# Optimization experiments

Hardware: AMD Instinct MI355X
Metric: run time of the kernel (lower is better)

Reference implementation:

```python
import jax, jax.numpy as jnp
import numpy as np

N, NPER, B, E = 65536, 1024, 64, 1048576
IN_F, HID, K, NCLS = 128, 64, 16, 10


def setup_inputs() -> dict:
    key = jax.random.key(0)
    ks = jax.random.split(key, 12)
    x = jax.random.normal(ks[0], (N, IN_F), jnp.float32)
    # block-structured intra-graph edges: 64 graphs of 1024 contiguous nodes
    gid = jax.random.randint(ks[1], (E,), 0, B)
    src = gid * NPER + jax.random.randint(ks[2], (E,), 0, NPER)
    dst = gid * NPER + jax.random.randint(ks[3], (E,), 0, NPER)
    edge_index = jnp.stack([src, dst]).astype(jnp.int32)
    batch = (jnp.arange(N, dtype=jnp.int32) // NPER).astype(jnp.int32)
    def lin(k, fo, fi):
        kw, kb = jax.random.split(k)
        s = 1.0 / np.sqrt(fi)
        return (jax.random.uniform(kw, (fo, fi), jnp.float32, -s, s),
                jax.random.uniform(kb, (fo,), jnp.float32, -s, s))
    W1, b1 = lin(ks[4], HID, IN_F)
    W2, b2 = lin(ks[5], HID, HID)
    Wp, bp = lin(ks[6], K, HID)      # DMoN cluster-assignment MLP (single Linear)
    Wl, bl = lin(ks[7], NCLS, HID)   # final classifier
    return {"x": x, "edge_index": edge_index, "batch": batch,
            "W1": W1, "b1": b1, "W2": W2, "b2": b2,
            "Wp": Wp, "bp": bp, "Wl": Wl, "bl": bl}


def gcn_conv(x, src, dst, W, b):
    # GCNConv with add_self_loops=True, symmetric normalization
    n = x.shape[0]
    deg = jax.ops.segment_sum(jnp.ones(src.shape[0], x.dtype), dst,
                              num_segments=n) + 1.0  # +1 for self-loop
    dinv = jax.lax.rsqrt(deg)
    h = x @ W.T
    coef = (dinv[src] * dinv[dst])[:, None]
    agg = jax.ops.segment_sum(h[src] * coef, dst, num_segments=n)
    agg = agg + h * (dinv * dinv)[:, None]  # self-loop contribution
    return agg + b


def reference(x, edge_index, batch, W1, b1, W2, b2, Wp, bp, Wl, bl):
    src, dst = edge_index[0], edge_index[1]
    h = jax.nn.relu(gcn_conv(x, src, dst, W1, b1))
    h = jax.nn.relu(gcn_conv(h, src, dst, W2, b2))
    # to_dense_batch: graphs are equal-sized and contiguous -> reshape, mask all True
    Xb = h.reshape(B, NPER, HID)
    # DMoN cluster assignment (dropout=0.0, mask all ones)
    s = jax.nn.softmax(Xb @ Wp.T + bp, axis=-1)          # [B, NPER, K]
    Xp = jax.nn.selu(jnp.einsum('bnk,bnh->bkh', s, Xb))   # pooled clusters [B, K, HID]
    out = Xp.mean(axis=1)                                  # [B, HID]
    logits = out @ Wl.T + bl                               # [B, NCLS]
    return logits
```

## Files before the change

### kernel.cpp

```cpp
#include <hip/hip_runtime.h>
#include <cstddef>

#define N_NODES 65536
#define NPER    1024
#define NGRAPH  64
#define HID     64
#define IN_F    128
#define KCLUS   16
#define NCLS    10
#define ECAP    20480
#define HSTRIDE 12
#define ZROW    NPER
#define LIN_BLOCKS 512

template <int K>
__device__ __forceinline__ void gemm_tile(const float* __restrict__ X,
                                          const float* __restrict__ W,
                                          float* __restrict__ Y,
                                          float (*xs)[68], float (*ws)[68],
                                          int block, int t) {
    const size_t row0 = (size_t)block * 128;
    const int rbase = t >> 3;
    const int cbase = t & 7;
    float acc[4][8] = {};

    for (int kc = 0; kc < K; kc += 64) {
        __syncthreads();
        for (int i = t; i < 128 * 16; i += 256) {
            int row = i >> 4, k4 = (i & 15) << 2;
            *(float4*)&xs[row][k4] = *(const float4*)(X + (row0 + row) * K + kc + k4);
        }
        for (int i = t; i < 64 * 16; i += 256) {
            int col = i >> 4, k4 = (i & 15) << 2;
            *(float4*)&ws[col][k4] = *(const float4*)(W + col * K + kc + k4);
        }
        __syncthreads();

#pragma unroll 4
        for (int k4 = 0; k4 < 64; k4 += 4) {
            float4 xr[4], wr[8];
#pragma unroll
            for (int rr = 0; rr < 4; ++rr) xr[rr] = *(const float4*)&xs[rbase + 32 * rr][k4];
#pragma unroll
            for (int cc = 0; cc < 8; ++cc) wr[cc] = *(const float4*)&ws[cbase + 8 * cc][k4];
#pragma unroll
            for (int rr = 0; rr < 4; ++rr)
#pragma unroll
                for (int cc = 0; cc < 8; ++cc) {
                    acc[rr][cc] = fmaf(xr[rr].x, wr[cc].x, acc[rr][cc]);
                    acc[rr][cc] = fmaf(xr[rr].y, wr[cc].y, acc[rr][cc]);
                    acc[rr][cc] = fmaf(xr[rr].z, wr[cc].z, acc[rr][cc]);
                    acc[rr][cc] = fmaf(xr[rr].w, wr[cc].w, acc[rr][cc]);
                }
        }
    }

#pragma unroll
    for (int rr = 0; rr < 4; ++rr)
#pragma unroll
        for (int cc = 0; cc < 8; ++cc)
            Y[(row0 + rbase + 32 * rr) * HID + cbase + 8 * cc] = acc[rr][cc];
}

__global__ __launch_bounds__(256) void front_kernel(const float* __restrict__ X,
                                                    const float* __restrict__ W,
                                                    float* __restrict__ Y,
                                                    const int* __restrict__ src,
                                                    const int* __restrict__ dst,
                                                    int* __restrict__ ecnt,
                                                    int* __restrict__ gedges, int E) {
    __shared__ float xs[128][68];
    __shared__ float ws[64][68];
    const int t = threadIdx.x;

    if (blockIdx.x >= LIN_BLOCKS) {
        int* hist = (int*)&xs[0][0];
        int* base_l = hist + NGRAPH;
        const int e0 = (blockIdx.x - LIN_BLOCKS) * 1024;
        if (t < NGRAPH) hist[t] = 0;
        __syncthreads();

        int gg[4], rr[4], pk[4];
#pragma unroll
        for (int i = 0; i < 4; ++i) {
            int idx = e0 + i * 256 + t;
            if (idx < E) {
                int d = dst[idx], s = src[idx];
                int g = d >> 10;
                gg[i] = g;
                pk[i] = ((d & 1023) << 10) | (s & 1023);
                rr[i] = atomicAdd(&hist[g], 1);
            } else gg[i] = -1;
        }
        __syncthreads();
        if (t < NGRAPH) base_l[t] = atomicAdd(&ecnt[t], hist[t]);
        __syncthreads();
#pragma unroll
        for (int i = 0; i < 4; ++i) {
            if (gg[i] >= 0) {
                int pos = base_l[gg[i]] + rr[i];
                if (pos < ECAP) gedges[gg[i] * ECAP + pos] = pk[i];
            }
        }
        return;
    }

    gemm_tile<IN_F>(X, W, Y, xs, ws, blockIdx.x, t);
}

template <int K>
__global__ __launch_bounds__(256) void linear_kernel(const float* __restrict__ X,
                                                     const float* __restrict__ W,
                                                     float* __restrict__ Y) {
    __shared__ float xs[128][68];
    __shared__ float ws[64][68];
    gemm_tile<K>(X, W, Y, xs, ws, blockIdx.x, threadIdx.x);
}

__global__ __launch_bounds__(1024) void scatter_kernel(const int* __restrict__ gedges,
                                                       const int* __restrict__ ecnt,
                                                       int* __restrict__ rp,
                                                       unsigned short* __restrict__ esorted,
                                                       float* __restrict__ dinv) {
    __shared__ int hist[NPER];
    __shared__ int wsum[16];
    const int g = blockIdx.x >> 3;
    const int sub = blockIdx.x & 7;
    const int t = threadIdx.x;
    const int lane = t & 63, wid = t >> 6;
    const int ec = ecnt[g];
    const int* ge = gedges + (size_t)g * ECAP;

    hist[t] = 0;
    __syncthreads();
    for (int i = t; i < ec; i += 1024) atomicAdd(&hist[ge[i] >> 10], 1);
    __syncthreads();

    const int h0 = hist[t];
    const int pd = (h0 + 3) & ~3;
    int v = pd;
#pragma unroll
    for (int off = 1; off < 64; off <<= 1) {
        int x = __shfl_up(v, off, 64);
        if (lane >= off) v += x;
    }
    if (lane == 63) wsum[wid] = v;
    __syncthreads();
    if (wid == 0) {
        int wv = (lane < 16) ? wsum[lane] : 0;
#pragma unroll
        for (int off = 1; off < 16; off <<= 1) {
            int x = __shfl_up(wv, off, 64);
            if (lane >= off) wv += x;
        }
        if (lane < 16) wsum[lane] = wv;
    }
    __syncthreads();
    const int incl = v + (wid > 0 ? wsum[wid - 1] : 0);
    const int excl = incl - pd;

    if (sub == 0) {
        rp[g * (NPER + 1) + t] = excl;
        if (t == NPER - 1) rp[g * (NPER + 1) + NPER] = incl;
        dinv[g * NPER + t] = rsqrtf((float)h0 + 1.0f);
    }
    __syncthreads();
    hist[t] = excl;
    __syncthreads();

    unsigned short* es = esorted + (size_t)g * ECAP;

    if ((t >> 7) == sub)
        for (int q = excl + h0; q < excl + pd; ++q) es[q] = (unsigned short)ZROW;

    for (int i = t; i < ec; i += 1024) {
        int pk = ge[i];
        int d = pk >> 10;
        if ((d >> 7) == sub) {
            int pos = atomicAdd(&hist[d], 1);
            es[pos] = (unsigned short)(pk & 1023);
        }
    }
}

__global__ __launch_bounds__(512) void agg_kernel(const float* __restrict__ h,
                                                  const unsigned short* __restrict__ esorted,
                                                  const int* __restrict__ rp,
                                                  const float* __restrict__ dinv,
                                                  const float* __restrict__ bias,
                                                  float* __restrict__ outp) {
    __shared__ float Hs[(NPER + 1) * HSTRIDE];
    __shared__ float dl[NPER];
    const int g = blockIdx.x & 63;
    const int f0 = (blockIdx.x >> 6) * 8;
    const int t = threadIdx.x;
    const int base = g * NPER;

    for (int r = t; r < NPER; r += 512) {
        const float* hp = h + (size_t)(base + r) * HID + f0;
        float4 a = *(const float4*)hp;
        float4 b = *(const float4*)(hp + 4);
        float dv = dinv[base + r];
        dl[r] = dv;
        float* row = &Hs[r * HSTRIDE];
        *(float4*)row = make_float4(a.x * dv, a.y * dv, a.z * dv, a.w * dv);
        *(float4*)(row + 4) = make_float4(b.x * dv, b.y * dv, b.z * dv, b.w * dv);
    }
    if (t < HSTRIDE) Hs[ZROW * HSTRIDE + t] = 0.f;
    float bb[8];
#pragma unroll
    for (int j = 0; j < 8; ++j) bb[j] = bias[f0 + j];
    const unsigned short* es = esorted + (size_t)g * ECAP;
    const int* rpg = rp + g * (NPER + 1);
    __syncthreads();

    for (int ld = t; ld < NPER; ld += 512) {
        int p = rpg[ld];
        const int pe = rpg[ld + 1];
        const float* srow = &Hs[ld * HSTRIDE];
        float4 acc0 = *(const float4*)srow;
        float4 acc1 = *(const float4*)(srow + 4);
        float4 bcc0 = make_float4(0.f, 0.f, 0.f, 0.f);
        float4 bcc1 = make_float4(0.f, 0.f, 0.f, 0.f);

        for (; p < pe; p += 4) {
            uint2 w4 = *(const uint2*)(es + p);
            const float* r0 = &Hs[(int)(w4.x & 0xFFFFu) * HSTRIDE];
            const float* r1 = &Hs[(int)(w4.x >> 16) * HSTRIDE];
            const float* r2 = &Hs[(int)(w4.y & 0xFFFFu) * HSTRIDE];
            const float* r3 = &Hs[(int)(w4.y >> 16) * HSTRIDE];
            float4 a0 = *(const float4*)r0, a1 = *(const float4*)(r0 + 4);
            float4 b0 = *(const float4*)r1, b1 = *(const float4*)(r1 + 4);
            float4 c0v = *(const float4*)r2, c1v = *(const float4*)(r2 + 4);
            float4 d0 = *(const float4*)r3, d1 = *(const float4*)(r3 + 4);
            acc0.x += a0.x; acc0.y += a0.y; acc0.z += a0.z; acc0.w += a0.w;
            acc1.x += a1.x; acc1.y += a1.y; acc1.z += a1.z; acc1.w += a1.w;
            bcc0.x += b0.x; bcc0.y += b0.y; bcc0.z += b0.z; bcc0.w += b0.w;
            bcc1.x += b1.x; bcc1.y += b1.y; bcc1.z += b1.z; bcc1.w += b1.w;
            acc0.x += c0v.x; acc0.y += c0v.y; acc0.z += c0v.z; acc0.w += c0v.w;
            acc1.x += c1v.x; acc1.y += c1v.y; acc1.z += c1v.z; acc1.w += c1v.w;
            bcc0.x += d0.x; bcc0.y += d0.y; bcc0.z += d0.z; bcc0.w += d0.w;
            bcc1.x += d1.x; bcc1.y += d1.y; bcc1.z += d1.z; bcc1.w += d1.w;
        }
        acc0.x += bcc0.x; acc0.y += bcc0.y; acc0.z += bcc0.z; acc0.w += bcc0.w;
        acc1.x += bcc1.x; acc1.y += bcc1.y; acc1.z += bcc1.z; acc1.w += bcc1.w;

        const float dv = dl[ld];
        float4 o0, o1;
        o0.x = fmaxf(fmaf(acc0.x, dv, bb[0]), 0.f);
        o0.y = fmaxf(fmaf(acc0.y, dv, bb[1]), 0.f);
        o0.z = fmaxf(fmaf(acc0.z, dv, bb[2]), 0.f);
        o0.w = fmaxf(fmaf(acc0.w, dv, bb[3]), 0.f);
        o1.x = fmaxf(fmaf(acc1.x, dv, bb[4]), 0.f);
        o1.y = fmaxf(fmaf(acc1.y, dv, bb[5]), 0.f);
        o1.z = fmaxf(fmaf(acc1.z, dv, bb[6]), 0.f);
        o1.w = fmaxf(fmaf(acc1.w, dv, bb[7]), 0.f);
        float* op = outp + (size_t)(base + ld) * HID + f0;
        *(float4*)op = o0;
        *(float4*)(op + 4) = o1;
    }
}

__global__ __launch_bounds__(256) void pool1_kernel(const float* __restrict__ h,
                                                    const float* __restrict__ Wp,
                                                    const float* __restrict__ bp,
                                                    float* __restrict__ xpart) {
    __shared__ float xs[128][HID + 1];
    __shared__ float ss[128][KCLUS + 1];
    __shared__ float wp[KCLUS][HID];
    __shared__ float bps[KCLUS];
    const int g = blockIdx.x >> 3;
    const int c = blockIdx.x & 7;
    const int t = threadIdx.x;
    const float* hb = h + ((size_t)g * NPER + c * 128) * HID;

    for (int i = t; i < 128 * HID / 4; i += 256) {
        float4 v = ((const float4*)hb)[i];
        int row = i >> 4, col = (i & 15) * 4;
        xs[row][col] = v.x; xs[row][col + 1] = v.y; xs[row][col + 2] = v.z; xs[row][col + 3] = v.w;
    }
    for (int i = t; i < KCLUS * HID; i += 256) wp[i >> 6][i & 63] = Wp[i];
    if (t < KCLUS) bps[t] = bp[t];
    __syncthreads();

    if (t < 128) {
        float lg[KCLUS];
        float mx = -1e30f;
#pragma unroll
        for (int k = 0; k < KCLUS; ++k) {
            float a = bps[k];
#pragma unroll 8
            for (int hh = 0; hh < HID; ++hh) a = fmaf(xs[t][hh], wp[k][hh], a);
            lg[k] = a;
            mx = fmaxf(mx, a);
        }
        float sum = 0.f;
#pragma unroll
        for (int k = 0; k < KCLUS; ++k) {
            lg[k] = __expf(lg[k] - mx);
            sum += lg[k];
        }
        float inv = 1.0f / sum;
#pragma unroll
        for (int k = 0; k < KCLUS; ++k) ss[t][k] = lg[k] * inv;
    }
    __syncthreads();

    const int hcol = t & 63;
    const int k0 = (t >> 6) * 4;
    float a0 = 0.f, a1 = 0.f, a2 = 0.f, a3 = 0.f;
#pragma unroll 8
    for (int n = 0; n < 128; ++n) {
        float xv = xs[n][hcol];
        a0 = fmaf(ss[n][k0 + 0], xv, a0);
        a1 = fmaf(ss[n][k0 + 1], xv, a1);
        a2 = fmaf(ss[n][k0 + 2], xv, a2);
        a3 = fmaf(ss[n][k0 + 3], xv, a3);
    }
    float* xp = xpart + (((size_t)(g * 8 + c)) * KCLUS + k0) * HID + hcol;
    xp[0] = a0; xp[HID] = a1; xp[2 * HID] = a2; xp[3 * HID] = a3;
}

__global__ __launch_bounds__(256) void pool2_kernel(const float* __restrict__ xpart,
                                                    const float* __restrict__ Wl,
                                                    const float* __restrict__ bl,
                                                    float* __restrict__ out) {
    __shared__ float xp[KCLUS][HID + 1];
    __shared__ float outm[HID];
    const int g = blockIdx.x;
    const int t = threadIdx.x;
    const int hcol = t & 63;
    const int k0 = (t >> 6) * 4;
    const float* base = xpart + (size_t)g * 8 * KCLUS * HID;

    float a[4] = {};
#pragma unroll
    for (int c = 0; c < 8; ++c)
#pragma unroll
        for (int j = 0; j < 4; ++j)
            a[j] += base[(c * KCLUS + k0 + j) * HID + hcol];

    const float sc = 1.0507009873554805f, al = 1.6732632423543772f;
#pragma unroll
    for (int j = 0; j < 4; ++j) {
        float v = a[j];
        xp[k0 + j][hcol] = v > 0.f ? sc * v : sc * al * (__expf(v) - 1.f);
    }
    __syncthreads();

    if (t < HID) {
        float m = 0.f;
#pragma unroll
        for (int k = 0; k < KCLUS; ++k) m += xp[k][t];
        outm[t] = m * (1.0f / KCLUS);
    }
    __syncthreads();

    if (t < NCLS) {
        float acc = bl[t];
#pragma unroll 8
        for (int hh = 0; hh < HID; ++hh) acc = fmaf(outm[hh], Wl[t * HID + hh], acc);
        out[g * NCLS + t] = acc;
    }
}

extern "C" void kernel_launch(void* const* d_in, const int* in_sizes, int n_in,
                              void* d_out, int out_size, void* d_ws, size_t ws_size,
                              hipStream_t stream) {
    const float* x  = (const float*)d_in[0];
    const int* eidx = (const int*)d_in[1];
    const float* W1 = (const float*)d_in[3];
    const float* b1 = (const float*)d_in[4];
    const float* W2 = (const float*)d_in[5];
    const float* b2 = (const float*)d_in[6];
    const float* Wp = (const float*)d_in[7];
    const float* bp = (const float*)d_in[8];
    const float* Wl = (const float*)d_in[9];
    const float* bl = (const float*)d_in[10];
    float* out = (float*)d_out;

    const int E = in_sizes[1] / 2;
    const int* src = eidx;
    const int* dst = eidx + E;

    char* w = (char*)d_ws;
    int*            ecnt    = (int*)w;            w += 256;
    int*            gedges  = (int*)w;            w += (size_t)NGRAPH * ECAP * 4;
    unsigned short* esorted = (unsigned short*)w; w += (size_t)NGRAPH * ECAP * 2;
    int*            rp      = (int*)w;            w += (size_t)NGRAPH * (NPER + 1) * 4;
    float*          dinv    = (float*)w;          w += (size_t)N_NODES * 4;
    float*          A       = (float*)w;          w += (size_t)N_NODES * HID * 4;
    float*          Bf      = (float*)w;          w += (size_t)N_NODES * HID * 4;
    float*          xpart   = (float*)w;          w += (size_t)NGRAPH * 8 * KCLUS * HID * 4;

    hipMemsetAsync(ecnt, 0, 256, stream);

    const int nbucket = (E + 1023) / 1024;
    front_kernel<<<LIN_BLOCKS + nbucket, 256, 0, stream>>>(x, W1, A, src, dst, ecnt, gedges, E);

    scatter_kernel<<<NGRAPH * 8, 1024, 0, stream>>>(gedges, ecnt, rp, esorted, dinv);

    agg_kernel<<<NGRAPH * 8, 512, 0, stream>>>(A, esorted, rp, dinv, b1, Bf);

    linear_kernel<HID><<<N_NODES / 128, 256, 0, stream>>>(Bf, W2, A);
    agg_kernel<<<NGRAPH * 8, 512, 0, stream>>>(A, esorted, rp, dinv, b2, Bf);

    pool1_kernel<<<NGRAPH * 8, 256, 0, stream>>>(Bf, Wp, bp, xpart);
    pool2_kernel<<<NGRAPH, 256, 0, stream>>>(xpart, Wl, bl, out);
}
```

Before: 218.0 us.

## Fuse node linear transforms into GCN aggregation kernels

Removes the standalone tiled GEMM kernels and computes each node's 8-feature slice of X·Wᵀ inside the aggregation kernel, just before staging it into shared memory. This drops the round trip of the transformed feature matrix through global memory and one kernel launch per layer. In exchange, each of the 8 feature-slice blocks per graph rereads the full input rows (128 or 64 floats per node), so input reads grow about eightfold. The GEMM also becomes a per-thread scalar dot-product loop with weights held in shared memory instead of a register-blocked tile.

```diff
diff --git a/kernel.cpp b/kernel.cpp
--- a/kernel.cpp
+++ b/kernel.cpp
@@ -11,110 +11,40 @@
 #define ECAP    20480
 #define HSTRIDE 12
 #define ZROW    NPER
-#define LIN_BLOCKS 512
-
-template <int K>
-__device__ __forceinline__ void gemm_tile(const float* __restrict__ X,
-                                          const float* __restrict__ W,
-                                          float* __restrict__ Y,
-                                          float (*xs)[68], float (*ws)[68],
-                                          int block, int t) {
-    const size_t row0 = (size_t)block * 128;
-    const int rbase = t >> 3;
-    const int cbase = t & 7;
-    float acc[4][8] = {};
-
-    for (int kc = 0; kc < K; kc += 64) {
-        __syncthreads();
-        for (int i = t; i < 128 * 16; i += 256) {
-            int row = i >> 4, k4 = (i & 15) << 2;
-            *(float4*)&xs[row][k4] = *(const float4*)(X + (row0 + row) * K + kc + k4);
-        }
-        for (int i = t; i < 64 * 16; i += 256) {
-            int col = i >> 4, k4 = (i & 15) << 2;
-            *(float4*)&ws[col][k4] = *(const float4*)(W + col * K + kc + k4);
-        }
-        __syncthreads();
-
-#pragma unroll 4
-        for (int k4 = 0; k4 < 64; k4 += 4) {
-            float4 xr[4], wr[8];
-#pragma unroll
-            for (int rr = 0; rr < 4; ++rr) xr[rr] = *(const float4*)&xs[rbase + 32 * rr][k4];
-#pragma unroll
-            for (int cc = 0; cc < 8; ++cc) wr[cc] = *(const float4*)&ws[cbase + 8 * cc][k4];
-#pragma unroll
-            for (int rr = 0; rr < 4; ++rr)
-#pragma unroll
-                for (int cc = 0; cc < 8; ++cc) {
-                    acc[rr][cc] = fmaf(xr[rr].x, wr[cc].x, acc[rr][cc]);
-                    acc[rr][cc] = fmaf(xr[rr].y, wr[cc].y, acc[rr][cc]);
-                    acc[rr][cc] = fmaf(xr[rr].z, wr[cc].z, acc[rr][cc]);
-                    acc[rr][cc] = fmaf(xr[rr].w, wr[cc].w, acc[rr][cc]);
-                }
-        }
-    }
-
-#pragma unroll
-    for (int rr = 0; rr < 4; ++rr)
-#pragma unroll
-        for (int cc = 0; cc < 8; ++cc)
-            Y[(row0 + rbase + 32 * rr) * HID + cbase + 8 * cc] = acc[rr][cc];
-}
-
-__global__ __launch_bounds__(256) void front_kernel(const float* __restrict__ X,
-                                                    const float* __restrict__ W,
-                                                    float* __restrict__ Y,
-                                                    const int* __restrict__ src,
-                                                    const int* __restrict__ dst,
-                                                    int* __restrict__ ecnt,
-                                                    int* __restrict__ gedges, int E) {
-    __shared__ float xs[128][68];
-    __shared__ float ws[64][68];
-    const int t = threadIdx.x;
-
-    if (blockIdx.x >= LIN_BLOCKS) {
-        int* hist = (int*)&xs[0][0];
-        int* base_l = hist + NGRAPH;
-        const int e0 = (blockIdx.x - LIN_BLOCKS) * 1024;
-        if (t < NGRAPH) hist[t] = 0;
-        __syncthreads();
-
-        int gg[4], rr[4], pk[4];
-#pragma unroll
-        for (int i = 0; i < 4; ++i) {
-            int idx = e0 + i * 256 + t;
-            if (idx < E) {
-                int d = dst[idx], s = src[idx];
-                int g = d >> 10;
-                gg[i] = g;
-                pk[i] = ((d & 1023) << 10) | (s & 1023);
-                rr[i] = atomicAdd(&hist[g], 1);
-            } else gg[i] = -1;
-        }
-        __syncthreads();
-        if (t < NGRAPH) base_l[t] = atomicAdd(&ecnt[t], hist[t]);
-        __syncthreads();
-#pragma unroll
-        for (int i = 0; i < 4; ++i) {
-            if (gg[i] >= 0) {
-                int pos = base_l[gg[i]] + rr[i];
-                if (pos < ECAP) gedges[gg[i] * ECAP + pos] = pk[i];
-            }
-        }
-        return;
-    }
-
-    gemm_tile<IN_F>(X, W, Y, xs, ws, blockIdx.x, t);
-}
-
-template <int K>
-__global__ __launch_bounds__(256) void linear_kernel(const float* __restrict__ X,
-                                                     const float* __restrict__ W,
-                                                     float* __restrict__ Y) {
-    __shared__ float xs[128][68];
-    __shared__ float ws[64][68];
-    gemm_tile<K>(X, W, Y, xs, ws, blockIdx.x, threadIdx.x);
+
+__global__ __launch_bounds__(256) void bucket_kernel(const int* __restrict__ src,
+                                                     const int* __restrict__ dst,
+                                                     int* __restrict__ ecnt,
+                                                     int* __restrict__ gedges, int E) {
+    __shared__ int hist[NGRAPH];
+    __shared__ int base_l[NGRAPH];
+    const int t = threadIdx.x;
+    const int e0 = blockIdx.x * 1024;
+    if (t < NGRAPH) hist[t] = 0;
+    __syncthreads();
+
+    int gg[4], rr[4], pk[4];
+#pragma unroll
+    for (int i = 0; i < 4; ++i) {
+        int idx = e0 + i * 256 + t;
+        if (idx < E) {
+            int d = dst[idx], s = src[idx];
+            int g = d >> 10;
+            gg[i] = g;
+            pk[i] = ((d & 1023) << 10) | (s & 1023);
+            rr[i] = atomicAdd(&hist[g], 1);
+        } else gg[i] = -1;
+    }
+    __syncthreads();
+    if (t < NGRAPH) base_l[t] = atomicAdd(&ecnt[t], hist[t]);
+    __syncthreads();
+#pragma unroll
+    for (int i = 0; i < 4; ++i) {
+        if (gg[i] >= 0) {
+            int pos = base_l[gg[i]] + rr[i];
+            if (pos < ECAP) gedges[gg[i] * ECAP + pos] = pk[i];
+        }
+    }
 }
 
 __global__ __launch_bounds__(1024) void scatter_kernel(const int* __restrict__ gedges,
@@ -183,28 +113,46 @@
     }
 }
 
-__global__ __launch_bounds__(512) void agg_kernel(const float* __restrict__ h,
-                                                  const unsigned short* __restrict__ esorted,
-                                                  const int* __restrict__ rp,
-                                                  const float* __restrict__ dinv,
-                                                  const float* __restrict__ bias,
-                                                  float* __restrict__ outp) {
+template <int K>
+__global__ __launch_bounds__(512, 4) void aggcsr_kernel(const float* __restrict__ X,
+                                                        const float* __restrict__ W,
+                                                        const float* __restrict__ bias,
+                                                        const unsigned short* __restrict__ esorted,
+                                                        const int* __restrict__ rp,
+                                                        const float* __restrict__ dinv,
+                                                        float* __restrict__ outp) {
     __shared__ float Hs[(NPER + 1) * HSTRIDE];
     __shared__ float dl[NPER];
+    __shared__ float wt[8][K];
     const int g = blockIdx.x & 63;
     const int f0 = (blockIdx.x >> 6) * 8;
     const int t = threadIdx.x;
     const int base = g * NPER;
 
+    for (int i = t; i < 8 * K; i += 512)
+        wt[i / K][i % K] = W[(size_t)(f0 + i / K) * K + (i % K)];
+    __syncthreads();
+
     for (int r = t; r < NPER; r += 512) {
-        const float* hp = h + (size_t)(base + r) * HID + f0;
-        float4 a = *(const float4*)hp;
-        float4 b = *(const float4*)(hp + 4);
+        const float* xr = X + (size_t)(base + r) * K;
+        float o[8] = {};
+#pragma unroll 4
+        for (int k = 0; k < K; k += 4) {
+            float4 xv = *(const float4*)(xr + k);
+#pragma unroll
+            for (int j = 0; j < 8; ++j) {
+                float4 wv = *(const float4*)&wt[j][k];
+                o[j] = fmaf(xv.x, wv.x, o[j]);
+                o[j] = fmaf(xv.y, wv.y, o[j]);
+                o[j] = fmaf(xv.z, wv.z, o[j]);
+                o[j] = fmaf(xv.w, wv.w, o[j]);
+            }
+        }
         float dv = dinv[base + r];
         dl[r] = dv;
         float* row = &Hs[r * HSTRIDE];
-        *(float4*)row = make_float4(a.x * dv, a.y * dv, a.z * dv, a.w * dv);
-        *(float4*)(row + 4) = make_float4(b.x * dv, b.y * dv, b.z * dv, b.w * dv);
+        *(float4*)row = make_float4(o[0] * dv, o[1] * dv, o[2] * dv, o[3] * dv);
+        *(float4*)(row + 4) = make_float4(o[4] * dv, o[5] * dv, o[6] * dv, o[7] * dv);
     }
     if (t < HSTRIDE) Hs[ZROW * HSTRIDE + t] = 0.f;
     float bb[8];
@@ -396,15 +344,14 @@
     hipMemsetAsync(ecnt, 0, 256, stream);
 
     const int nbucket = (E + 1023) / 1024;
-    front_kernel<<<LIN_BLOCKS + nbucket, 256, 0, stream>>>(x, W1, A, src, dst, ecnt, gedges, E);
+    bucket_kernel<<<nbucket, 256, 0, stream>>>(src, dst, ecnt, gedges, E);
 
     scatter_kernel<<<NGRAPH * 8, 1024, 0, stream>>>(gedges, ecnt, rp, esorted, dinv);
 
-    agg_kernel<<<NGRAPH * 8, 512, 0, stream>>>(A, esorted, rp, dinv, b1, Bf);
-
-    linear_kernel<HID><<<N_NODES / 128, 256, 0, stream>>>(Bf, W2, A);
-    agg_kernel<<<NGRAPH * 8, 512, 0, stream>>>(A, esorted, rp, dinv, b2, Bf);
-
-    pool1_kernel<<<NGRAPH * 8, 256, 0, stream>>>(Bf, Wp, bp, xpart);
+    aggcsr_kernel<IN_F><<<NGRAPH * 8, 512, 0, stream>>>(x, W1, b1, esorted, rp, dinv, Bf);
+
+    aggcsr_kernel<HID><<<NGRAPH * 8, 512, 0, stream>>>(Bf, W2, b2, esorted, rp, dinv, A);
+
+    pool1_kernel<<<NGRAPH * 8, 256, 0, stream>>>(A, Wp, bp, xpart);
     pool2_kernel<<<NGRAPH, 256, 0, stream>>>(xpart, Wl, bl, out);
 }
```

New measurement: 230.3 us. 5.7% more time.

## Gather neighbor features directly from global memory instead of LDS staging

Applied to the files above, without the earlier changes.

The aggregation kernel no longer stages pre-scaled feature slices of each graph into shared memory. Each thread now owns one destination node and 16 features, gathers neighbor rows straight from global/L2, and scales each by the neighbor's dinv loaded per edge. This drops the LDS fill and the block barrier and halves the number of blocks. In exchange every edge costs uncached-LDS global loads and an extra dinv gather, plus more registers per thread.

```diff
diff --git a/kernel.cpp b/kernel.cpp
--- a/kernel.cpp
+++ b/kernel.cpp
@@ -9,7 +9,6 @@
 #define KCLUS   16
 #define NCLS    10
 #define ECAP    20480
-#define HSTRIDE 12
 #define ZROW    NPER
 #define LIN_BLOCKS 512
 
@@ -183,82 +182,115 @@
     }
 }
 
-__global__ __launch_bounds__(512) void agg_kernel(const float* __restrict__ h,
-                                                  const unsigned short* __restrict__ esorted,
-                                                  const int* __restrict__ rp,
-                                                  const float* __restrict__ dinv,
-                                                  const float* __restrict__ bias,
-                                                  float* __restrict__ outp) {
-    __shared__ float Hs[(NPER + 1) * HSTRIDE];
-    __shared__ float dl[NPER];
+__global__ __launch_bounds__(1024) void agg_kernel(const float* __restrict__ h,
+                                                   const unsigned short* __restrict__ esorted,
+                                                   const int* __restrict__ rp,
+                                                   const float* __restrict__ dinv,
+                                                   const float* __restrict__ bias,
+                                                   float* __restrict__ outp) {
     const int g = blockIdx.x & 63;
-    const int f0 = (blockIdx.x >> 6) * 8;
-    const int t = threadIdx.x;
+    const int f0 = (blockIdx.x >> 6) * 16;
+    const int r = threadIdx.x;
     const int base = g * NPER;
-
-    for (int r = t; r < NPER; r += 512) {
-        const float* hp = h + (size_t)(base + r) * HID + f0;
-        float4 a = *(const float4*)hp;
-        float4 b = *(const float4*)(hp + 4);
-        float dv = dinv[base + r];
-        dl[r] = dv;
-        float* row = &Hs[r * HSTRIDE];
-        *(float4*)row = make_float4(a.x * dv, a.y * dv, a.z * dv, a.w * dv);
-        *(float4*)(row + 4) = make_float4(b.x * dv, b.y * dv, b.z * dv, b.w * dv);
-    }
-    if (t < HSTRIDE) Hs[ZROW * HSTRIDE + t] = 0.f;
-    float bb[8];
-#pragma unroll
-    for (int j = 0; j < 8; ++j) bb[j] = bias[f0 + j];
+    const float* __restrict__ hb = h + (size_t)base * HID + f0;
+    const float* __restrict__ dvg = dinv + base;
+
+    const float dv = dvg[r];
+    const float* own = hb + (size_t)r * HID;
+    float4 acc0 = *(const float4*)(own);
+    float4 acc1 = *(const float4*)(own + 4);
+    float4 acc2 = *(const float4*)(own + 8);
+    float4 acc3 = *(const float4*)(own + 12);
+    acc0.x *= dv; acc0.y *= dv; acc0.z *= dv; acc0.w *= dv;
+    acc1.x *= dv; acc1.y *= dv; acc1.z *= dv; acc1.w *= dv;
+    acc2.x *= dv; acc2.y *= dv; acc2.z *= dv; acc2.w *= dv;
+    acc3.x *= dv; acc3.y *= dv; acc3.z *= dv; acc3.w *= dv;
+
     const unsigned short* es = esorted + (size_t)g * ECAP;
     const int* rpg = rp + g * (NPER + 1);
-    __syncthreads();
-
-    for (int ld = t; ld < NPER; ld += 512) {
-        int p = rpg[ld];
-        const int pe = rpg[ld + 1];
-        const float* srow = &Hs[ld * HSTRIDE];
-        float4 acc0 = *(const float4*)srow;
-        float4 acc1 = *(const float4*)(srow + 4);
-        float4 bcc0 = make_float4(0.f, 0.f, 0.f, 0.f);
-        float4 bcc1 = make_float4(0.f, 0.f, 0.f, 0.f);
-
-        for (; p < pe; p += 4) {
-            uint2 w4 = *(const uint2*)(es + p);
-            const float* r0 = &Hs[(int)(w4.x & 0xFFFFu) * HSTRIDE];
-            const float* r1 = &Hs[(int)(w4.x >> 16) * HSTRIDE];
-            const float* r2 = &Hs[(int)(w4.y & 0xFFFFu) * HSTRIDE];
-            const float* r3 = &Hs[(int)(w4.y >> 16) * HSTRIDE];
-            float4 a0 = *(const float4*)r0, a1 = *(const float4*)(r0 + 4);
-            float4 b0 = *(const float4*)r1, b1 = *(const float4*)(r1 + 4);
-            float4 c0v = *(const float4*)r2, c1v = *(const float4*)(r2 + 4);
-            float4 d0 = *(const float4*)r3, d1 = *(const float4*)(r3 + 4);
-            acc0.x += a0.x; acc0.y += a0.y; acc0.z += a0.z; acc0.w += a0.w;
-            acc1.x += a1.x; acc1.y += a1.y; acc1.z += a1.z; acc1.w += a1.w;
-            bcc0.x += b0.x; bcc0.y += b0.y; bcc0.z += b0.z; bcc0.w += b0.w;
-            bcc1.x += b1.x; bcc1.y += b1.y; bcc1.z += b1.z; bcc1.w += b1.w;
-            acc0.x += c0v.x; acc0.y += c0v.y; acc0.z += c0v.z; acc0.w += c0v.w;
-            acc1.x += c1v.x; acc1.y += c1v.y; acc1.z += c1v.z; acc1.w += c1v.w;
-            bcc0.x += d0.x; bcc0.y += d0.y; bcc0.z += d0.z; bcc0.w += d0.w;
-            bcc1.x += d1.x; bcc1.y += d1.y; bcc1.z += d1.z; bcc1.w += d1.w;
-        }
-        acc0.x += bcc0.x; acc0.y += bcc0.y; acc0.z += bcc0.z; acc0.w += bcc0.w;
-        acc1.x += bcc1.x; acc1.y += bcc1.y; acc1.z += bcc1.z; acc1.w += bcc1.w;
-
-        const float dv = dl[ld];
-        float4 o0, o1;
-        o0.x = fmaxf(fmaf(acc0.x, dv, bb[0]), 0.f);
-        o0.y = fmaxf(fmaf(acc0.y, dv, bb[1]), 0.f);
-        o0.z = fmaxf(fmaf(acc0.z, dv, bb[2]), 0.f);
-        o0.w = fmaxf(fmaf(acc0.w, dv, bb[3]), 0.f);
-        o1.x = fmaxf(fmaf(acc1.x, dv, bb[4]), 0.f);
-        o1.y = fmaxf(fmaf(acc1.y, dv, bb[5]), 0.f);
-        o1.z = fmaxf(fmaf(acc1.z, dv, bb[6]), 0.f);
-        o1.w = fmaxf(fmaf(acc1.w, dv, bb[7]), 0.f);
-        float* op = outp + (size_t)(base + ld) * HID + f0;
-        *(float4*)op = o0;
-        *(float4*)(op + 4) = o1;
-    }
+    int p = rpg[r];
+    const int pe = rpg[r + 1];
+
+    for (; p < pe; p += 4) {
+        uint2 w4 = *(const uint2*)(es + p);
+        int s0 = (int)(w4.x & 0xFFFFu), s1 = (int)(w4.x >> 16);
+        int s2 = (int)(w4.y & 0xFFFFu), s3 = (int)(w4.y >> 16);
+        int i0 = s0 < NPER ? s0 : 0, i1 = s1 < NPER ? s1 : 0;
+        int i2 = s2 < NPER ? s2 : 0, i3 = s3 < NPER ? s3 : 0;
+        float c0 = s0 < NPER ? dvg[i0] : 0.f;
+        float c1 = s1 < NPER ? dvg[i1] : 0.f;
+        float c2 = s2 < NPER ? dvg[i2] : 0.f;
+        float c3 = s3 < NPER ? dvg[i3] : 0.f;
+        const float* q0 = hb + (size_t)i0 * HID;
+        const float* q1 = hb + (size_t)i1 * HID;
+        const float* q2 = hb + (size_t)i2 * HID;
+        const float* q3 = hb + (size_t)i3 * HID;
+        float4 a00 = *(const float4*)(q0),     a01 = *(const float4*)(q0 + 4);
+        float4 a02 = *(const float4*)(q0 + 8), a03 = *(const float4*)(q0 + 12);
+        float4 b00 = *(const float4*)(q1),     b01 = *(const float4*)(q1 + 4);
+        float4 b02 = *(const float4*)(q1 + 8), b03 = *(const float4*)(q1 + 12);
+        float4 c00 = *(const float4*)(q2),     c01 = *(const float4*)(q2 + 4);
+        float4 c02 = *(const float4*)(q2 + 8), c03 = *(const float4*)(q2 + 12);
+        float4 d00 = *(const float4*)(q3),     d01 = *(const float4*)(q3 + 4);
+        float4 d02 = *(const float4*)(q3 + 8), d03 = *(const float4*)(q3 + 12);
+
+        acc0.x = fmaf(a00.x, c0, acc0.x); acc0.y = fmaf(a00.y, c0, acc0.y);
+        acc0.z = fmaf(a00.z, c0, acc0.z); acc0.w = fmaf(a00.w, c0, acc0.w);
+        acc1.x = fmaf(a01.x, c0, acc1.x); acc1.y = fmaf(a01.y, c0, acc1.y);
+        acc1.z = fmaf(a01.z, c0, acc1.z); acc1.w = fmaf(a01.w, c0, acc1.w);
+        acc2.x = fmaf(a02.x, c0, acc2.x); acc2.y = fmaf(a02.y, c0, acc2.y);
+        acc2.z = fmaf(a02.z, c0, acc2.z); acc2.w = fmaf(a02.w, c0, acc2.w);
+        acc3.x = fmaf(a03.x, c0, acc3.x); acc3.y = fmaf(a03.y, c0, acc3.y);
+        acc3.z = fmaf(a03.z, c0, acc3.z); acc3.w = fmaf(a03.w, c0, acc3.w);
+
+        acc0.x = fmaf(b00.x, c1, acc0.x); acc0.y = fmaf(b00.y, c1, acc0.y);
+        acc0.z = fmaf(b00.z, c1, acc0.z); acc0.w = fmaf(b00.w, c1, acc0.w);
+        acc1.x = fmaf(b01.x, c1, acc1.x); acc1.y = fmaf(b01.y, c1, acc1.y);
+        acc1.z = fmaf(b01.z, c1, acc1.z); acc1.w = fmaf(b01.w, c1, acc1.w);
+        acc2.x = fmaf(b02.x, c1, acc2.x); acc2.y = fmaf(b02.y, c1, acc2.y);
+        acc2.z = fmaf(b02.z, c1, acc2.z); acc2.w = fmaf(b02.w, c1, acc2.w);
+        acc3.x = fmaf(b03.x, c1, acc3.x); acc3.y = fmaf(b03.y, c1, acc3.y);
+        acc3.z = fmaf(b03.z, c1, acc3.z); acc3.w = fmaf(b03.w, c1, acc3.w);
+
+        acc0.x = fmaf(c00.x, c2, acc0.x); acc0.y = fmaf(c00.y, c2, acc0.y);
+        acc0.z = fmaf(c00.z, c2, acc0.z); acc0.w = fmaf(c00.w, c2, acc0.w);
+        acc1.x = fmaf(c01.x, c2, acc1.x); acc1.y = fmaf(c01.y, c2, acc1.y);
+        acc1.z = fmaf(c01.z, c2, acc1.z); acc1.w = fmaf(c01.w, c2, acc1.w);
+        acc2.x = fmaf(c02.x, c2, acc2.x); acc2.y = fmaf(c02.y, c2, acc2.y);
+        acc2.z = fmaf(c02.z, c2, acc2.z); acc2.w = fmaf(c02.w, c2, acc2.w);
+        acc3.x = fmaf(c03.x, c2, acc3.x); acc3.y = fmaf(c03.y, c2, acc3.y);
+        acc3.z = fmaf(c03.z, c2, acc3.z); acc3.w = fmaf(c03.w, c2, acc3.w);
+
+        acc0.x = fmaf(d00.x, c3, acc0.x); acc0.y = fmaf(d00.y, c3, acc0.y);
+        acc0.z = fmaf(d00.z, c3, acc0.z); acc0.w = fmaf(d00.w, c3, acc0.w);
+        acc1.x = fmaf(d01.x, c3, acc1.x); acc1.y = fmaf(d01.y, c3, acc1.y);
+        acc1.z = fmaf(d01.z, c3, acc1.z); acc1.w = fmaf(d01.w, c3, acc1.w);
+        acc2.x = fmaf(d02.x, c3, acc2.x); acc2.y = fmaf(d02.y, c3, acc2.y);
+        acc2.z = fmaf(d02.z, c3, acc2.z); acc2.w = fmaf(d02.w, c3, acc2.w);
+        acc3.x = fmaf(d03.x, c3, acc3.x); acc3.y = fmaf(d03.y, c3, acc3.y);
+        acc3.z = fmaf(d03.z, c3, acc3.z); acc3.w = fmaf(d03.w, c3, acc3.w);
+    }
+
+    float4 bb0 = *(const float4*)(bias + f0);
+    float4 bb1 = *(const float4*)(bias + f0 + 4);
+    float4 bb2 = *(const float4*)(bias + f0 + 8);
+    float4 bb3 = *(const float4*)(bias + f0 + 12);
+
+    float4 o0, o1, o2, o3;
+    o0.x = fmaxf(fmaf(acc0.x, dv, bb0.x), 0.f); o0.y = fmaxf(fmaf(acc0.y, dv, bb0.y), 0.f);
+    o0.z = fmaxf(fmaf(acc0.z, dv, bb0.z), 0.f); o0.w = fmaxf(fmaf(acc0.w, dv, bb0.w), 0.f);
+    o1.x = fmaxf(fmaf(acc1.x, dv, bb1.x), 0.f); o1.y = fmaxf(fmaf(acc1.y, dv, bb1.y), 0.f);
+    o1.z = fmaxf(fmaf(acc1.z, dv, bb1.z), 0.f); o1.w = fmaxf(fmaf(acc1.w, dv, bb1.w), 0.f);
+    o2.x = fmaxf(fmaf(acc2.x, dv, bb2.x), 0.f); o2.y = fmaxf(fmaf(acc2.y, dv, bb2.y), 0.f);
+    o2.z = fmaxf(fmaf(acc2.z, dv, bb2.z), 0.f); o2.w = fmaxf(fmaf(acc2.w, dv, bb2.w), 0.f);
+    o3.x = fmaxf(fmaf(acc3.x, dv, bb3.x), 0.f); o3.y = fmaxf(fmaf(acc3.y, dv, bb3.y), 0.f);
+    o3.z = fmaxf(fmaf(acc3.z, dv, bb3.z), 0.f); o3.w = fmaxf(fmaf(acc3.w, dv, bb3.w), 0.f);
+
+    float* op = outp + (size_t)(base + r) * HID + f0;
+    *(float4*)(op)      = o0;
+    *(float4*)(op + 4)  = o1;
+    *(float4*)(op + 8)  = o2;
+    *(float4*)(op + 12) = o3;
 }
 
 __global__ __launch_bounds__(256) void pool1_kernel(const float* __restrict__ h,
@@ -400,10 +432,10 @@
 
     scatter_kernel<<<NGRAPH * 8, 1024, 0, stream>>>(gedges, ecnt, rp, esorted, dinv);
 
-    agg_kernel<<<NGRAPH * 8, 512, 0, stream>>>(A, esorted, rp, dinv, b1, Bf);
+    agg_kernel<<<NGRAPH * 4, 1024, 0, stream>>>(A, esorted, rp, dinv, b1, Bf);
 
     linear_kernel<HID><<<N_NODES / 128, 256, 0, stream>>>(Bf, W2, A);
-    agg_kernel<<<NGRAPH * 8, 512, 0, stream>>>(A, esorted, rp, dinv, b2, Bf);
+    agg_kernel<<<NGRAPH * 4, 1024, 0, stream>>>(A, esorted, rp, dinv, b2, Bf);
 
     pool1_kernel<<<NGRAPH * 8, 256, 0, stream>>>(Bf, Wp, bp, xpart);
     pool2_kernel<<<NGRAPH, 256, 0, stream>>>(xpart, Wl, bl, out);
```

Result: slower. 277.7 us (+27.4%).
